# Kernel optimization log

Hardware: AMD Instinct MI355X
Metric: run time of the kernel (lower is better)

Reference implementation:

```python
import jax, jax.numpy as jnp
import numpy as np

EMBED_DIM = 1024
NUM_HEADS = 16
HEAD_DIM = EMBED_DIM // NUM_HEADS
B, T = 2, 2048


def setup_inputs() -> dict:
    key = jax.random.key(0)
    ks = jax.random.split(key, 10)
    s_in = 1.0 / np.sqrt(EMBED_DIM)
    s_hd = 1.0 / np.sqrt(HEAD_DIM)
    return {
        "hidden_states": jax.random.normal(ks[0], (B, T, EMBED_DIM), jnp.float32),
        "attn_mask": jnp.zeros((T, T), jnp.float32),
        # per-head parameter stacks (nn.Linear: y = x @ W^T + b); store W pre-transposed
        "W_q": jax.random.uniform(ks[1], (NUM_HEADS, EMBED_DIM, HEAD_DIM), jnp.float32, -s_in, s_in),
        "b_q": jax.random.uniform(ks[2], (NUM_HEADS, HEAD_DIM), jnp.float32, -s_in, s_in),
        "W_k": jax.random.uniform(ks[3], (NUM_HEADS, EMBED_DIM, HEAD_DIM), jnp.float32, -s_in, s_in),
        "b_k": jax.random.uniform(ks[4], (NUM_HEADS, HEAD_DIM), jnp.float32, -s_in, s_in),
        "W_v": jax.random.uniform(ks[5], (NUM_HEADS, EMBED_DIM, HEAD_DIM), jnp.float32, -s_in, s_in),
        "b_v": jax.random.uniform(ks[6], (NUM_HEADS, HEAD_DIM), jnp.float32, -s_in, s_in),
        "W_o": jax.random.uniform(ks[7], (NUM_HEADS, HEAD_DIM, EMBED_DIM), jnp.float32, -s_hd, s_hd),
        "b_o": jax.random.uniform(ks[8], (NUM_HEADS, EMBED_DIM), jnp.float32, -s_hd, s_hd),
        "gate": jnp.ones((NUM_HEADS,), jnp.float32),
    }


def reference(hidden_states, attn_mask, W_q, b_q, W_k, b_k, W_v, b_v, W_o, b_o, gate):
    # All heads: state='active', consent=True (defaults); dropout in eval mode.
    scale = 1.0 / np.sqrt(HEAD_DIM)
    # Q,K,V: [B,H,T,hd]
    Q = jnp.einsum("btd,hde->bhte", hidden_states, W_q) + b_q[None, :, None, :]
    K = jnp.einsum("btd,hde->bhte", hidden_states, W_k) + b_k[None, :, None, :]
    V = jnp.einsum("btd,hde->bhte", hidden_states, W_v) + b_v[None, :, None, :]
    scores = jnp.einsum("bhte,bhse->bhts", Q, K) * scale + attn_mask[None, None, :, :]
    weights = jax.nn.softmax(scores, axis=-1)
    out = jnp.einsum("bhts,bhse->bhte", weights, V)  # [B,H,T,hd]
    # per-head scalar norm: mean over (B,T) of L2 norm along head_dim, floored at 1e-5
    denom = jnp.maximum(
        jnp.sqrt(jnp.sum(out * out, axis=-1)).mean(axis=(0, 2)), 1e-5
    )  # [H]
    out_n = out / denom[None, :, None, None]
    g = jnp.clip(gate, 0.0, 1.0)  # gate_factor = 1.0 for 'active' heads
    # projected per head: (out_n @ W_o + b_o) * g; then sum over heads / H
    proj = (jnp.einsum("bhte,hed->bhtd", out_n, W_o) + b_o[None, :, None, :]) * g[None, :, None, None]
    return proj.sum(axis=1) / NUM_HEADS
```

## Files before the change

### kernel.cpp

```cpp
#include <hip/hip_runtime.h>
#include <hip/hip_bf16.h>
#include <math.h>

#define EMBED_DIM 1024
#define NUM_HEADS 16
#define HEAD_DIM  64
#define B_SZ      2
#define T_SZ      2048
#define BT        (B_SZ * T_SZ)
#define LOG2E     1.44269504088896340736f
#define QSCALE    (0.125f * LOG2E)
#define SOFT_OFF  8.0f

typedef short bf16x8 __attribute__((ext_vector_type(8)));
typedef float f32x4  __attribute__((ext_vector_type(4)));

#define MFMA16(a, b, c) __builtin_amdgcn_mfma_f32_16x16x32_bf16((a), (b), (c), 0, 0, 0)

__device__ inline short f2bf(float f) {
    unsigned u = __builtin_bit_cast(unsigned, f);
    u = (u + 0x7fffu + ((u >> 16) & 1u)) >> 16;
    return (short)u;
}
__device__ inline float bf2f(short s) {
    unsigned u = ((unsigned)(unsigned short)s) << 16;
    return __builtin_bit_cast(float, u);
}
__device__ inline unsigned pk2(float a, float b) {
#if __has_builtin(__builtin_amdgcn_cvt_pk_bf16_f32)
    typedef __bf16 bf2_t __attribute__((ext_vector_type(2)));
    bf2_t t = __builtin_amdgcn_cvt_pk_bf16_f32(a, b);
    return __builtin_bit_cast(unsigned, t);
#else
    return (unsigned)(unsigned short)f2bf(a) | ((unsigned)(unsigned short)f2bf(b) << 16);
#endif
}

__device__ inline void gld16(const short* g, short* lds) {
    __builtin_amdgcn_global_load_lds(
        (const __attribute__((address_space(1))) void*)g,
        (__attribute__((address_space(3))) void*)lds, 16, 0, 0);
}

__device__ inline bf16x8 frag_swz(const short* tile, int R, int C) {
    return *(const bf16x8*)(tile + R * 64 + ((C ^ (R & 7)) << 3));
}

__device__ inline float red_add64(float v) {
    v += __shfl_xor(v, 1); v += __shfl_xor(v, 2); v += __shfl_xor(v, 4);
    v += __shfl_xor(v, 8); v += __shfl_xor(v, 16); v += __shfl_xor(v, 32);
    return v;
}

__global__ __launch_bounds__(256) void cvt_in_kernel(
    const float* __restrict__ hs, short* __restrict__ hsb)
{
    const long i = ((long)blockIdx.x * 256 + threadIdx.x) * 4;
    const float4 v = *(const float4*)(hs + i);
    ushort4 o; o.x = f2bf(v.x); o.y = f2bf(v.y); o.z = f2bf(v.z); o.w = f2bf(v.w);
    *(ushort4*)(hsb + i) = o;
}

__global__ __launch_bounds__(256) void transpose_w_kernel(
    const float* __restrict__ Wq, const float* __restrict__ Wk,
    const float* __restrict__ Wv, const float* __restrict__ Wo,
    short* __restrict__ Wqt, short* __restrict__ Wkt,
    short* __restrict__ Wvt, short* __restrict__ WoT)
{
    const int arr = blockIdx.z, h = blockIdx.y;
    const float* src; short* dst; int R, C;
    if (arr == 0)      { src = Wq; dst = Wqt; R = 1024; C = 64; }
    else if (arr == 1) { src = Wk; dst = Wkt; R = 1024; C = 64; }
    else if (arr == 2) { src = Wv; dst = Wvt; R = 1024; C = 64; }
    else               { src = Wo; dst = WoT; R = 64;   C = 1024; }
    src += (long)h * 65536; dst += (long)h * 65536;

    const int ct = C / 32;
    const int tr = blockIdx.x / ct, tc = blockIdx.x % ct;
    __shared__ float tile[32][33];
    const int tx = threadIdx.x & 31, ty = threadIdx.x >> 5;
    #pragma unroll
    for (int i = 0; i < 4; ++i) {
        const int r = ty + 8 * i;
        tile[r][tx] = src[(long)(tr * 32 + r) * C + tc * 32 + tx];
    }
    __syncthreads();
    #pragma unroll
    for (int i = 0; i < 4; ++i) {
        const int r = ty + 8 * i;
        dst[(long)(tc * 32 + r) * R + tr * 32 + tx] = f2bf(tile[tx][r]);
    }
}

__global__ __launch_bounds__(256) void qkv_mfma_kernel(
    const short* __restrict__ hsb,
    const short* __restrict__ Wt,
    const float* __restrict__ bq, const float* __restrict__ bk,
    const float* __restrict__ bv,
    short* __restrict__ Qb, short* __restrict__ Kb, short* __restrict__ Vtb)
{
    const int m0 = blockIdx.x * 128;
    const int n0 = blockIdx.y * 128;
    __shared__ short As[128 * 64];
    __shared__ short Bs[128 * 64];

    const int tid = threadIdx.x, lane = tid & 63, w = tid >> 6;
    const int wm = w & 1, wn = w >> 1;
    const int quad = lane >> 4, l15 = lane & 15;

    f32x4 acc[4][4] = {};

    for (int k0 = 0; k0 < 1024; k0 += 64) {
        __syncthreads();
        #pragma unroll
        for (int t = 0; t < 4; ++t) {
            const int r0 = w * 32 + t * 8;
            const int r  = r0 + (lane >> 3);
            const int cg = (lane & 7) ^ (r & 7);
            gld16(hsb + (long)(m0 + r) * 1024 + k0 + cg * 8, &As[r0 * 64]);
            gld16(Wt  + (long)(n0 + r) * 1024 + k0 + cg * 8, &Bs[r0 * 64]);
        }
        __syncthreads();
        #pragma unroll
        for (int ks = 0; ks < 2; ++ks) {
            bf16x8 af[4];
            #pragma unroll
            for (int ms = 0; ms < 4; ++ms)
                af[ms] = frag_swz(As, wm * 64 + ms * 16 + l15, ks * 4 + quad);
            #pragma unroll
            for (int ns = 0; ns < 4; ++ns) {
                const bf16x8 bfr = frag_swz(Bs, wn * 64 + ns * 16 + l15, ks * 4 + quad);
                #pragma unroll
                for (int ms = 0; ms < 4; ++ms)
                    acc[ms][ns] = MFMA16(af[ms], bfr, acc[ms][ns]);
            }
        }
    }

    #pragma unroll
    for (int ns = 0; ns < 4; ++ns) {
        const int n    = n0 + wn * 64 + ns * 16 + l15;
        const int type = n >> 10;
        const int h    = (n >> 6) & 15;
        const int e    = n & 63;
        const float bias = (type == 0 ? bq : type == 1 ? bk : bv)[h * 64 + e];
        #pragma unroll
        for (int ms = 0; ms < 4; ++ms) {
            const int mbase = m0 + wm * 64 + ms * 16 + quad * 4;
            const int bb = mbase >> 11, t0 = mbase & 2047;
            if (type == 2) {
                const int tp = (t0 & ~63) | (t0 & 35) | ((t0 & 12) << 1) | ((t0 & 16) >> 2);
                ushort4 pk;
                pk.x = (unsigned short)f2bf(acc[ms][ns][0] + bias);
                pk.y = (unsigned short)f2bf(acc[ms][ns][1] + bias);
                pk.z = (unsigned short)f2bf(acc[ms][ns][2] + bias);
                pk.w = (unsigned short)f2bf(acc[ms][ns][3] + bias);
                *(ushort4*)&Vtb[((long)(bb * 16 + h) * 64 + e) * 2048 + tp] = pk;
            } else {
                #pragma unroll
                for (int r = 0; r < 4; ++r) {
                    const float v = acc[ms][ns][r] + bias;
                    const long off = ((long)(bb * 16 + h) * 2048 + (t0 + r)) * 64 + e;
                    if (type == 0) Qb[off] = f2bf(v * QSCALE);
                    else           Kb[off] = f2bf(v);
                }
            }
        }
    }
}

__global__ __launch_bounds__(256) void attn_mfma_kernel(
    const short* __restrict__ Qb, const short* __restrict__ Kb,
    const short* __restrict__ Vtb, const float* __restrict__ maskf,
    short* __restrict__ Ob, float* __restrict__ denomsum)
{
    const int q0 = blockIdx.x * 128;
    const int h  = blockIdx.y, b = blockIdx.z;
    const long bh = ((long)b * 16 + h) * (long)T_SZ * 64;

    __shared__ short Ks[2][64 * 64];
    __shared__ short Vs[2][64 * 64];
    __shared__ float wred[4];

    const int tid = threadIdx.x, lane = tid & 63, w = tid >> 6;
    const int quad = lane >> 4, l15 = lane & 15;
    const int qrowA = q0 + w * 32 + l15;

    const short* Kg = Kb + bh;
    const short* Vg = Vtb + bh;

    bf16x8 qf[2][2];
    #pragma unroll
    for (int qs = 0; qs < 2; ++qs)
        #pragma unroll
        for (int ks = 0; ks < 2; ++ks)
            qf[qs][ks] = *(const bf16x8*)(Qb + bh +
                (long)(qrowA + qs * 16) * 64 + ks * 32 + quad * 8);

    f32x4 o[2][4] = {};
    float lp[2] = {0.f, 0.f};

    const float* mrowA = maskf + (long)qrowA * 2048 + quad * 4;

    auto stageKV = [&](int kt, int buf) {
        const int kv0 = kt * 64;
        #pragma unroll
        for (int t = 0; t < 2; ++t) {
            const int r0 = w * 16 + t * 8;
            const int r  = r0 + (lane >> 3);
            const int cg = (lane & 7) ^ (r & 7);
            gld16(Kg + (long)(kv0 + r) * 64 + cg * 8, &Ks[buf][r0 * 64]);
            gld16(Vg + (long)r * 2048 + kv0 + cg * 8, &Vs[buf][r0 * 64]);
        }
    };

    float4 mv[2][4];
    auto loadMask = [&](int kt) {
        const int kv0 = kt * 64;
        #pragma unroll
        for (int qs = 0; qs < 2; ++qs)
            #pragma unroll
            for (int kb = 0; kb < 4; ++kb)
                mv[qs][kb] = *(const float4*)(mrowA + (long)qs * 16 * 2048 + kv0 + kb * 16);
    };

    stageKV(0, 0);
    loadMask(0);

    for (int kt = 0; kt < 32; ++kt) {
        const int cur = kt & 1;

        __builtin_amdgcn_s_barrier();
        asm volatile("" ::: "memory");
        if (kt < 31) {
            stageKV(kt + 1, cur ^ 1);
            asm volatile("s_waitcnt vmcnt(4)" ::: "memory");
        } else {
            asm volatile("s_waitcnt vmcnt(0)" ::: "memory");
        }
        __builtin_amdgcn_s_barrier();
        asm volatile("" ::: "memory");

        f32x4 s[2][4];
        #pragma unroll
        for (int qs = 0; qs < 2; ++qs)
            #pragma unroll
            for (int kb = 0; kb < 4; ++kb) {
                s[qs][kb][0] = fmaf(mv[qs][kb].x, LOG2E, -SOFT_OFF);
                s[qs][kb][1] = fmaf(mv[qs][kb].y, LOG2E, -SOFT_OFF);
                s[qs][kb][2] = fmaf(mv[qs][kb].z, LOG2E, -SOFT_OFF);
                s[qs][kb][3] = fmaf(mv[qs][kb].w, LOG2E, -SOFT_OFF);
            }

        bf16x8 kf[2][4];
        #pragma unroll
        for (int ks = 0; ks < 2; ++ks)
            #pragma unroll
            for (int kb = 0; kb < 4; ++kb)
                kf[ks][kb] = frag_swz(&Ks[cur][0], kb * 16 + l15, ks * 4 + quad);

        __builtin_amdgcn_s_setprio(1);
        #pragma unroll
        for (int qs = 0; qs < 2; ++qs)
            #pragma unroll
            for (int ks = 0; ks < 2; ++ks)
                #pragma unroll
                for (int kb = 0; kb < 4; ++kb)
                    s[qs][kb] = MFMA16(kf[ks][kb], qf[qs][ks], s[qs][kb]);
        __builtin_amdgcn_s_setprio(0);

        if (kt < 31) loadMask(kt + 1);

        unsigned w0[2][4], w1[2][4];
        #pragma unroll
        for (int qs = 0; qs < 2; ++qs) {
            float rs = 0.f;
            #pragma unroll
            for (int kb = 0; kb < 4; ++kb) {
                const float p0 = exp2f(s[qs][kb][0]);
                const float p1 = exp2f(s[qs][kb][1]);
                const float p2 = exp2f(s[qs][kb][2]);
                const float p3 = exp2f(s[qs][kb][3]);
                rs += (p0 + p1) + (p2 + p3);
                w0[qs][kb] = pk2(p0, p1);
                w1[qs][kb] = pk2(p2, p3);
            }
            lp[qs] += rs;
        }

        bf16x8 va[2][4];
        #pragma unroll
        for (int kbp = 0; kbp < 2; ++kbp)
            #pragma unroll
            for (int eb = 0; eb < 4; ++eb)
                va[kbp][eb] = frag_swz(&Vs[cur][0], eb * 16 + l15, kbp * 4 + quad);

        __builtin_amdgcn_s_setprio(1);
        #pragma unroll
        for (int qs = 0; qs < 2; ++qs)
            #pragma unroll
            for (int kbp = 0; kbp < 2; ++kbp) {
                const uint4 u = {w0[qs][2 * kbp], w1[qs][2 * kbp],
                                 w0[qs][2 * kbp + 1], w1[qs][2 * kbp + 1]};
                const bf16x8 pb = __builtin_bit_cast(bf16x8, u);
                #pragma unroll
                for (int eb = 0; eb < 4; ++eb)
                    o[qs][eb] = MFMA16(va[kbp][eb], pb, o[qs][eb]);
            }
        __builtin_amdgcn_s_setprio(0);
    }

    float tot = 0.f;
    #pragma unroll
    for (int qs = 0; qs < 2; ++qs) {
        float lf = lp[qs];
        lf += __shfl_xor(lf, 16);
        lf += __shfl_xor(lf, 32);
        const float inv = 1.f / lf;
        float ss = 0.f;
        #pragma unroll
        for (int eb = 0; eb < 4; ++eb) {
            o[qs][eb] *= inv;
            #pragma unroll
            for (int r = 0; r < 4; ++r) ss += o[qs][eb][r] * o[qs][eb][r];
        }
        ss += __shfl_xor(ss, 16);
        ss += __shfl_xor(ss, 32);
        tot += sqrtf(ss);

        const int qrow = qrowA + qs * 16;
        #pragma unroll
        for (int eb = 0; eb < 4; ++eb) {
            uint2 pk;
            pk.x = pk2(o[qs][eb][0], o[qs][eb][1]);
            pk.y = pk2(o[qs][eb][2], o[qs][eb][3]);
            *(uint2*)&Ob[((long)(b * 2048 + qrow)) * 1024 + h * 64 + eb * 16 + quad * 4] = pk;
        }
    }
    const float wsum = red_add64(tot) * 0.25f;
    if (lane == 0) wred[w] = wsum;
    __syncthreads();
    if (tid == 0)
        atomicAdd(&denomsum[h], wred[0] + wred[1] + wred[2] + wred[3]);
}

__global__ __launch_bounds__(256) void scale_w_kernel(
    short* __restrict__ WoT, const float* __restrict__ denomsum,
    const float* __restrict__ gate)
{
    __shared__ float sh[16];
    if (threadIdx.x < 16) {
        const float g  = fminf(fmaxf(gate[threadIdx.x], 0.f), 1.f);
        const float dn = fmaxf(denomsum[threadIdx.x] * (1.f / (float)BT), 1e-5f);
        sh[threadIdx.x] = g / (dn * (float)NUM_HEADS);
    }
    __syncthreads();
    const long i = ((long)blockIdx.x * 256 + threadIdx.x) * 4;
    const float sc = sh[(int)(i >> 16)];
    ushort4 v = *(ushort4*)(WoT + i);
    v.x = (unsigned short)f2bf(bf2f((short)v.x) * sc);
    v.y = (unsigned short)f2bf(bf2f((short)v.y) * sc);
    v.z = (unsigned short)f2bf(bf2f((short)v.z) * sc);
    v.w = (unsigned short)f2bf(bf2f((short)v.w) * sc);
    *(ushort4*)(WoT + i) = v;
}

__global__ __launch_bounds__(256) void oproj_mfma_kernel(
    const short* __restrict__ Ob,
    const short* __restrict__ WoT,
    const float* __restrict__ bo,
    const float* __restrict__ gate,
    float* __restrict__ out)
{
    const int m0 = blockIdx.x * 128;
    const int n0 = blockIdx.y * 128;
    __shared__ short As[2][128 * 64];
    __shared__ short Bs[2][128 * 64];

    const int tid = threadIdx.x, lane = tid & 63, w = tid >> 6;
    const int wm = w & 1, wn = w >> 1;
    const int quad = lane >> 4, l15 = lane & 15;

    auto stage = [&](int h, int buf) {
        #pragma unroll
        for (int t = 0; t < 4; ++t) {
            const int r0 = w * 32 + t * 8;
            const int r  = r0 + (lane >> 3);
            const int cg = (lane & 7) ^ (r & 7);
            gld16(Ob + (long)(m0 + r) * 1024 + h * 64 + cg * 8, &As[buf][r0 * 64]);
            gld16(WoT + (long)h * 65536 + (long)(n0 + r) * 64 + cg * 8, &Bs[buf][r0 * 64]);
        }
    };

    f32x4 acc[4][4] = {};
    stage(0, 0);

    for (int h = 0; h < 16; ++h) {
        const int cur = h & 1;
        __syncthreads();
        if (h < 15) stage(h + 1, cur ^ 1);
        #pragma unroll
        for (int ks = 0; ks < 2; ++ks) {
            bf16x8 af[4];
            #pragma unroll
            for (int ms = 0; ms < 4; ++ms)
                af[ms] = frag_swz(&As[cur][0], wm * 64 + ms * 16 + l15, ks * 4 + quad);
            #pragma unroll
            for (int ns = 0; ns < 4; ++ns) {
                const bf16x8 bfr = frag_swz(&Bs[cur][0], wn * 64 + ns * 16 + l15, ks * 4 + quad);
                #pragma unroll
                for (int ms = 0; ms < 4; ++ms)
                    acc[ms][ns] = MFMA16(af[ms], bfr, acc[ms][ns]);
            }
        }
    }

    float gcl[16];
    #pragma unroll
    for (int hh = 0; hh < 16; ++hh)
        gcl[hh] = fminf(fmaxf(gate[hh], 0.f), 1.f) * (1.f / (float)NUM_HEADS);

    #pragma unroll
    for (int ns = 0; ns < 4; ++ns) {
        const int n = n0 + wn * 64 + ns * 16 + l15;
        float be = 0.f;
        #pragma unroll
        for (int hh = 0; hh < 16; ++hh) be += gcl[hh] * bo[hh * 1024 + n];
        #pragma unroll
        for (int ms = 0; ms < 4; ++ms) {
            const int m = m0 + wm * 64 + ms * 16 + quad * 4;
            #pragma unroll
            for (int r = 0; r < 4; ++r)
                out[(long)(m + r) * 1024 + n] = acc[ms][ns][r] + be;
        }
    }
}

extern "C" void kernel_launch(void* const* d_in, const int* in_sizes, int n_in,
                              void* d_out, int out_size, void* d_ws, size_t ws_size,
                              hipStream_t stream)
{
    const float* hs   = (const float*)d_in[0];
    const float* mask = (const float*)d_in[1];
    const float* Wq   = (const float*)d_in[2];
    const float* bq   = (const float*)d_in[3];
    const float* Wk   = (const float*)d_in[4];
    const float* bk   = (const float*)d_in[5];
    const float* Wv   = (const float*)d_in[6];
    const float* bv   = (const float*)d_in[7];
    const float* Wo   = (const float*)d_in[8];
    const float* bo   = (const float*)d_in[9];
    const float* gate = (const float*)d_in[10];
    float* out = (float*)d_out;

    char* ws = (char*)d_ws;
    const size_t MB = 1024 * 1024;
    short* hsb   = (short*)(ws);
    short* Wqt   = (short*)(ws + 8  * MB);
    short* Wkt   = (short*)(ws + 10 * MB);
    short* Wvt   = (short*)(ws + 12 * MB);
    short* WoT   = (short*)(ws + 14 * MB);
    short* Qb    = (short*)(ws + 16 * MB);
    short* Kb    = (short*)(ws + 24 * MB);
    short* Vtb   = (short*)(ws + 32 * MB);
    short* Ob    = (short*)(ws + 40 * MB);
    float* denomsum = (float*)(ws + 48 * MB);

    (void)hipMemsetAsync(denomsum, 0, NUM_HEADS * sizeof(float), stream);

    cvt_in_kernel<<<4096, 256, 0, stream>>>(hs, hsb);
    transpose_w_kernel<<<dim3(64, 16, 4), 256, 0, stream>>>(
        Wq, Wk, Wv, Wo, Wqt, Wkt, Wvt, WoT);
    qkv_mfma_kernel<<<dim3(32, 24), 256, 0, stream>>>(
        hsb, Wqt, bq, bk, bv, Qb, Kb, Vtb);
    attn_mfma_kernel<<<dim3(16, 16, 2), 256, 0, stream>>>(
        Qb, Kb, Vtb, mask, Ob, denomsum);
    scale_w_kernel<<<1024, 256, 0, stream>>>(WoT, denomsum, gate);
    oproj_mfma_kernel<<<dim3(32, 8), 256, 0, stream>>>(
        Ob, WoT, bo, gate, out);
}
```

Baseline: 262.5 us.

## Split attention KV range across two blocks and add a combine kernel

Attention blocks now grow to 512 threads covering 256 query rows, and each block handles only half of the KV sequence (split-K style), writing unnormalized partial outputs and row sums. A new combine kernel merges the two halves, normalizes, writes Ob, and accumulates the per-head norm sum. It also drops the s_setprio hints and switches to the raw hardware exp2 builtin. The goal is to shorten each block's serial KV loop and raise occupancy, at the cost of an extra kernel launch, additional bf16 partial-output traffic, and precision loss from storing unnormalized partials in bf16.

```diff
diff --git a/kernel.cpp b/kernel.cpp
--- a/kernel.cpp
+++ b/kernel.cpp
@@ -36,6 +36,14 @@
 #endif
 }
 
+__device__ inline float ex2(float x) {
+#if __has_builtin(__builtin_amdgcn_exp2f)
+    return __builtin_amdgcn_exp2f(x);
+#else
+    return exp2f(x);
+#endif
+}
+
 __device__ inline void gld16(const short* g, short* lds) {
     __builtin_amdgcn_global_load_lds(
         (const __attribute__((address_space(1))) void*)g,
@@ -44,12 +52,6 @@
 
 __device__ inline bf16x8 frag_swz(const short* tile, int R, int C) {
     return *(const bf16x8*)(tile + R * 64 + ((C ^ (R & 7)) << 3));
-}
-
-__device__ inline float red_add64(float v) {
-    v += __shfl_xor(v, 1); v += __shfl_xor(v, 2); v += __shfl_xor(v, 4);
-    v += __shfl_xor(v, 8); v += __shfl_xor(v, 16); v += __shfl_xor(v, 32);
-    return v;
 }
 
 __global__ __launch_bounds__(256) void cvt_in_kernel(
@@ -169,18 +171,21 @@
     }
 }
 
-__global__ __launch_bounds__(256) void attn_mfma_kernel(
+__global__ __launch_bounds__(512) void attn_mfma_kernel(
     const short* __restrict__ Qb, const short* __restrict__ Kb,
     const short* __restrict__ Vtb, const float* __restrict__ maskf,
-    short* __restrict__ Ob, float* __restrict__ denomsum)
-{
-    const int q0 = blockIdx.x * 128;
+    short* __restrict__ Opart,
+    float* __restrict__ lpart)
+{
+    const int qc   = blockIdx.x >> 1;
+    const int half = blockIdx.x & 1;
+    const int q0 = qc * 256;
     const int h  = blockIdx.y, b = blockIdx.z;
     const long bh = ((long)b * 16 + h) * (long)T_SZ * 64;
+    const int kvbase = half * 1024;
 
     __shared__ short Ks[2][64 * 64];
     __shared__ short Vs[2][64 * 64];
-    __shared__ float wred[4];
 
     const int tid = threadIdx.x, lane = tid & 63, w = tid >> 6;
     const int quad = lane >> 4, l15 = lane & 15;
@@ -200,18 +205,15 @@
     f32x4 o[2][4] = {};
     float lp[2] = {0.f, 0.f};
 
-    const float* mrowA = maskf + (long)qrowA * 2048 + quad * 4;
+    const float* mrowA = maskf + (long)qrowA * 2048 + kvbase + quad * 4;
 
     auto stageKV = [&](int kt, int buf) {
-        const int kv0 = kt * 64;
-        #pragma unroll
-        for (int t = 0; t < 2; ++t) {
-            const int r0 = w * 16 + t * 8;
-            const int r  = r0 + (lane >> 3);
-            const int cg = (lane & 7) ^ (r & 7);
-            gld16(Kg + (long)(kv0 + r) * 64 + cg * 8, &Ks[buf][r0 * 64]);
-            gld16(Vg + (long)r * 2048 + kv0 + cg * 8, &Vs[buf][r0 * 64]);
-        }
+        const int kv0 = kvbase + kt * 64;
+        const int r0 = w * 8;
+        const int r  = r0 + (lane >> 3);
+        const int cg = (lane & 7) ^ (r & 7);
+        gld16(Kg + (long)(kv0 + r) * 64 + cg * 8, &Ks[buf][r0 * 64]);
+        gld16(Vg + (long)r * 2048 + kv0 + cg * 8, &Vs[buf][r0 * 64]);
     };
 
     float4 mv[2][4];
@@ -227,14 +229,14 @@
     stageKV(0, 0);
     loadMask(0);
 
-    for (int kt = 0; kt < 32; ++kt) {
+    for (int kt = 0; kt < 16; ++kt) {
         const int cur = kt & 1;
 
         __builtin_amdgcn_s_barrier();
         asm volatile("" ::: "memory");
-        if (kt < 31) {
+        if (kt < 15) {
             stageKV(kt + 1, cur ^ 1);
-            asm volatile("s_waitcnt vmcnt(4)" ::: "memory");
+            asm volatile("s_waitcnt vmcnt(2)" ::: "memory");
         } else {
             asm volatile("s_waitcnt vmcnt(0)" ::: "memory");
         }
@@ -259,7 +261,6 @@
             for (int kb = 0; kb < 4; ++kb)
                 kf[ks][kb] = frag_swz(&Ks[cur][0], kb * 16 + l15, ks * 4 + quad);
 
-        __builtin_amdgcn_s_setprio(1);
         #pragma unroll
         for (int qs = 0; qs < 2; ++qs)
             #pragma unroll
@@ -267,9 +268,8 @@
                 #pragma unroll
                 for (int kb = 0; kb < 4; ++kb)
                     s[qs][kb] = MFMA16(kf[ks][kb], qf[qs][ks], s[qs][kb]);
-        __builtin_amdgcn_s_setprio(0);
-
-        if (kt < 31) loadMask(kt + 1);
+
+        if (kt < 15) loadMask(kt + 1);
 
         unsigned w0[2][4], w1[2][4];
         #pragma unroll
@@ -277,10 +277,10 @@
             float rs = 0.f;
             #pragma unroll
             for (int kb = 0; kb < 4; ++kb) {
-                const float p0 = exp2f(s[qs][kb][0]);
-                const float p1 = exp2f(s[qs][kb][1]);
-                const float p2 = exp2f(s[qs][kb][2]);
-                const float p3 = exp2f(s[qs][kb][3]);
+                const float p0 = ex2(s[qs][kb][0]);
+                const float p1 = ex2(s[qs][kb][1]);
+                const float p2 = ex2(s[qs][kb][2]);
+                const float p3 = ex2(s[qs][kb][3]);
                 rs += (p0 + p1) + (p2 + p3);
                 w0[qs][kb] = pk2(p0, p1);
                 w1[qs][kb] = pk2(p2, p3);
@@ -295,7 +295,6 @@
             for (int eb = 0; eb < 4; ++eb)
                 va[kbp][eb] = frag_swz(&Vs[cur][0], eb * 16 + l15, kbp * 4 + quad);
 
-        __builtin_amdgcn_s_setprio(1);
         #pragma unroll
         for (int qs = 0; qs < 2; ++qs)
             #pragma unroll
@@ -307,41 +306,61 @@
                 for (int eb = 0; eb < 4; ++eb)
                     o[qs][eb] = MFMA16(va[kbp][eb], pb, o[qs][eb]);
             }
-        __builtin_amdgcn_s_setprio(0);
-    }
-
-    float tot = 0.f;
+    }
+
     #pragma unroll
     for (int qs = 0; qs < 2; ++qs) {
         float lf = lp[qs];
         lf += __shfl_xor(lf, 16);
         lf += __shfl_xor(lf, 32);
-        const float inv = 1.f / lf;
-        float ss = 0.f;
-        #pragma unroll
-        for (int eb = 0; eb < 4; ++eb) {
-            o[qs][eb] *= inv;
-            #pragma unroll
-            for (int r = 0; r < 4; ++r) ss += o[qs][eb][r] * o[qs][eb][r];
-        }
-        ss += __shfl_xor(ss, 16);
-        ss += __shfl_xor(ss, 32);
-        tot += sqrtf(ss);
-
         const int qrow = qrowA + qs * 16;
+        const long rbase = (long)b * 2048 + qrow;
         #pragma unroll
         for (int eb = 0; eb < 4; ++eb) {
             uint2 pk;
             pk.x = pk2(o[qs][eb][0], o[qs][eb][1]);
             pk.y = pk2(o[qs][eb][2], o[qs][eb][3]);
-            *(uint2*)&Ob[((long)(b * 2048 + qrow)) * 1024 + h * 64 + eb * 16 + quad * 4] = pk;
-        }
-    }
-    const float wsum = red_add64(tot) * 0.25f;
-    if (lane == 0) wred[w] = wsum;
+            *(uint2*)&Opart[(long)half * (4096 * 1024) + rbase * 1024 +
+                            h * 64 + eb * 16 + quad * 4] = pk;
+        }
+        if (quad == 0)
+            lpart[(long)half * (4096 * 16) + rbase * 16 + h] = lf;
+    }
+}
+
+__global__ __launch_bounds__(256) void combine_kernel(
+    const short* __restrict__ Opart,
+    const float* __restrict__ lpart,
+    short* __restrict__ Ob,
+    float* __restrict__ denomsum)
+{
+    __shared__ float hacc[16];
+    const int tid = threadIdx.x;
+    if (tid < 16) hacc[tid] = 0.f;
     __syncthreads();
-    if (tid == 0)
-        atomicAdd(&denomsum[h], wred[0] + wred[1] + wred[2] + wred[3]);
+    const int h = tid >> 4;
+    const int row0 = blockIdx.x * 16;
+    for (int rr = 0; rr < 16; ++rr) {
+        const int row = row0 + rr;
+        const long base = (long)row * 1024 + tid * 4;
+        const ushort4 a0 = *(const ushort4*)(Opart + base);
+        const ushort4 a1 = *(const ushort4*)(Opart + (long)4096 * 1024 + base);
+        const float l0 = lpart[row * 16 + h];
+        const float l1 = lpart[4096 * 16 + row * 16 + h];
+        const float inv = 1.f / (l0 + l1);
+        const float o0 = (bf2f((short)a0.x) + bf2f((short)a1.x)) * inv;
+        const float o1 = (bf2f((short)a0.y) + bf2f((short)a1.y)) * inv;
+        const float o2 = (bf2f((short)a0.z) + bf2f((short)a1.z)) * inv;
+        const float o3 = (bf2f((short)a0.w) + bf2f((short)a1.w)) * inv;
+        uint2 pk; pk.x = pk2(o0, o1); pk.y = pk2(o2, o3);
+        *(uint2*)(Ob + base) = pk;
+        float ss = (o0 * o0 + o1 * o1) + (o2 * o2 + o3 * o3);
+        ss += __shfl_xor(ss, 1); ss += __shfl_xor(ss, 2);
+        ss += __shfl_xor(ss, 4); ss += __shfl_xor(ss, 8);
+        if ((tid & 15) == 0) atomicAdd(&hacc[h], sqrtf(ss));
+    }
+    __syncthreads();
+    if (tid < 16) atomicAdd(&denomsum[tid], hacc[tid]);
 }
 
 __global__ __launch_bounds__(256) void scale_w_kernel(
@@ -459,12 +478,14 @@
     short* Wqt   = (short*)(ws + 8  * MB);
     short* Wkt   = (short*)(ws + 10 * MB);
     short* Wvt   = (short*)(ws + 12 * MB);
-    short* WoT   = (short*)(ws + 14 * MB);
+    short* Opart = (short*)(ws);
     short* Qb    = (short*)(ws + 16 * MB);
     short* Kb    = (short*)(ws + 24 * MB);
     short* Vtb   = (short*)(ws + 32 * MB);
     short* Ob    = (short*)(ws + 40 * MB);
-    float* denomsum = (float*)(ws + 48 * MB);
+    short* WoT   = (short*)(ws + 48 * MB);
+    float* lpart = (float*)(ws + 50 * MB);
+    float* denomsum = (float*)(ws + 51 * MB);
 
     (void)hipMemsetAsync(denomsum, 0, NUM_HEADS * sizeof(float), stream);
 
@@ -473,8 +494,9 @@
         Wq, Wk, Wv, Wo, Wqt, Wkt, Wvt, WoT);
     qkv_mfma_kernel<<<dim3(32, 24), 256, 0, stream>>>(
         hsb, Wqt, bq, bk, bv, Qb, Kb, Vtb);
-    attn_mfma_kernel<<<dim3(16, 16, 2), 256, 0, stream>>>(
-        Qb, Kb, Vtb, mask, Ob, denomsum);
+    attn_mfma_kernel<<<dim3(16, 16, 2), 512, 0, stream>>>(
+        Qb, Kb, Vtb, mask, Opart, lpart);
+    combine_kernel<<<256, 256, 0, stream>>>(Opart, lpart, Ob, denomsum);
     scale_w_kernel<<<1024, 256, 0, stream>>>(WoT, denomsum, gate);
     oproj_mfma_kernel<<<dim3(32, 8), 256, 0, stream>>>(
         Ob, WoT, bo, gate, out);
```

Measured after the change: 282.9 us. 1.08x slower.
